# Optimization experiments

Hardware: AMD Instinct MI355X
Metric: run time of the kernel (lower is better)

Reference implementation:

```python
import jax, jax.numpy as jnp
import numpy as np

# dims
T, B, NB, P = 128, 8, 256, 16
N = NB * P            # 4096 neurons
E = 4096              # active block-edges (target_connectivity=16 per block)
# cfg constants
ACT_LR = 0.01         # homeostatic bias learning rate
SETPOINT = 0.1        # homeostatic activity setpoint
SYN_LR = 0.01         # synaptic learning rate
ALPHA = 0.01          # trophic map EMA alpha
MAX_NORM = 1.0        # per-block weight norm cap
DMAX = 0.1            # per-block delta norm cap
EPS = 1e-8


def setup_inputs() -> dict:
    key = jax.random.key(0)
    ks = jax.random.split(key, 10)
    return {
        "states": jax.random.normal(ks[0], (T, B, N), jnp.float32),
        "elig": jax.random.normal(ks[1], (T, B, N), jnp.float32),
        "act": jax.random.uniform(ks[2], (T, B, N), jnp.float32),
        "inv": jax.random.uniform(ks[3], (T, B, 1), jnp.float32),
        "var": jax.random.normal(ks[4], (T, B, N), jnp.float32),
        "weight_values": jax.random.normal(ks[5], (E, P, P), jnp.float32) * 0.1,
        "activity_bias": jax.random.normal(ks[6], (1, N), jnp.float32) * 0.01,
        "trophic_map": jax.random.uniform(ks[7], (NB, NB), jnp.float32),
        "weight_rows": jax.random.randint(ks[8], (E,), 0, NB, jnp.int32),
        "weight_cols": jax.random.randint(ks[9], (E,), 0, NB, jnp.int32),
        "active_blocks": jnp.ones((E,), jnp.bool_),
    }


def reference(states, elig, act, inv, var, weight_values, activity_bias,
              trophic_map, weight_rows, weight_cols, active_blocks):
    mask = active_blocks.astype(weight_values.dtype)  # [E]

    def step(carry, xs):
        W, bias, troph = carry
        s, e, a, iv, v = xs  # s,e,a,v: [B,N]; iv: [B,1]
        # 1) homeostatic bias update toward setpoint
        bias = bias + ACT_LR * jnp.mean((SETPOINT - a) * iv, axis=0, keepdims=True)
        # 2) modulated error signal with postsynaptic gain (1 - s^2)
        mod = v * (1.0 - s * s)                         # [B,N]
        eb = e.reshape(B, NB, P)                        # eligibility pre blocks
        mb = mod.reshape(B, NB, P)                      # modulated post blocks
        pre = eb[:, weight_cols]                        # [B,E,P] gather
        post = mb[:, weight_rows]                       # [B,E,P] gather
        ivb = iv[:, 0]                                  # [B]
        # 3) Hebbian outer product (norm-scaled, batch-averaged) minus Oja decay
        hebb = jnp.einsum('bei,bej,b->eij', post, pre, ivb) / B   # [E,P,P]
        post2 = jnp.einsum('bei,b->ei', post * post, ivb) / B     # [E,P]
        dw = hebb - post2[:, :, None] * W
        # clip per-block update norm (delta_max_norm)
        dn = jnp.sqrt(jnp.sum(dw * dw, axis=(1, 2), keepdims=True))
        dw = dw * jnp.minimum(1.0, DMAX / (dn + EPS))
        W = W + SYN_LR * dw * mask[:, None, None]
        # renormalize per-block weight norm (max_norm)
        wn = jnp.sqrt(jnp.sum(W * W, axis=(1, 2), keepdims=True))
        W = W * jnp.minimum(1.0, MAX_NORM / (wn + EPS))
        # 4) trophic support map EMA via scatter of per-edge update strength
        strength = jnp.sqrt(jnp.sum(dw * dw, axis=(1, 2)))         # [E]
        troph = (1.0 - ALPHA) * troph
        troph = troph.at[weight_rows, weight_cols].add(ALPHA * strength)
        return (W, bias, troph), None

    (W, bias, troph), _ = jax.lax.scan(
        step, (weight_values, activity_bias, trophic_map),
        (states, elig, act, inv, var))
    return W
```

## Files before the change

### kernel.cpp

```cpp
#include <hip/hip_runtime.h>


namespace {
constexpr int T = 128, B = 8, NB = 256, P = 16;
constexpr int N = NB * P;
constexpr int E = 4096;
constexpr int BN = B * N;
constexpr float SYN_LR = 0.01f;
constexpr float DMAX   = 0.1f;
}

typedef __attribute__((ext_vector_type(8))) short short8v;
typedef __attribute__((ext_vector_type(4))) float float4v;
typedef __attribute__((ext_vector_type(2))) float float2v;

#if defined(__HIP_DEVICE_COMPILE__)
#define MFMA_B16(A, Bv, C) \
  __builtin_amdgcn_mfma_f32_16x16x32_bf16((A), (Bv), (C), 0, 0, 0)
#else
static __device__ inline float4v MFMA_B16(short8v, short8v, float4v C) { return C; }
#endif

__device__ __forceinline__ uint32_t bf16_rne(float x) {
  const uint32_t u = __float_as_uint(x);
  return (u + 0x7fffu + ((u >> 16) & 1u)) >> 16;
}

template<int CTRL>
__device__ __forceinline__ float dpp_add(float v) {
  return v + __int_as_float(__builtin_amdgcn_update_dpp(
      0, __float_as_int(v), CTRL, 0xF, 0xF, true));
}
__device__ __forceinline__ float wave_total(float v) {
  v = dpp_add<0xB1>(v);
  v = dpp_add<0x4E>(v);
  v = dpp_add<0x141>(v);
  v = dpp_add<0x140>(v);
  v = dpp_add<0x142>(v);
  v = dpp_add<0x143>(v);
  return __int_as_float(__builtin_amdgcn_readlane(__float_as_int(v), 63));
}

__global__ __launch_bounds__(256)
void prepass2(const float* __restrict__ states,
              const float* __restrict__ var,
              const float* __restrict__ elig,
              const float* __restrict__ inv,
              uint4* __restrict__ postT,
              uint4* __restrict__ preT,
              float* __restrict__ postSq)
{
  const int t  = blockIdx.x >> 2;
  const int n4 = ((blockIdx.x & 3) << 8) | threadIdx.x;
  const int n0 = n4 * 4;
  const size_t base = (size_t)t * BN + n0;

  uint32_t ph[4][4], pl[4][4], qh[4][4];
  float sq[4] = {0.f, 0.f, 0.f, 0.f};
#pragma unroll
  for (int b = 0; b < 8; ++b) {
    const float sc = sqrtf(inv[t * B + b] * 0.125f);
    const float4 s4 = *reinterpret_cast<const float4*>(states + base + (size_t)b * N);
    const float4 v4 = *reinterpret_cast<const float4*>(var    + base + (size_t)b * N);
    const float4 e4 = *reinterpret_cast<const float4*>(elig   + base + (size_t)b * N);
    const float ss[4] = {s4.x, s4.y, s4.z, s4.w};
    const float vv[4] = {v4.x, v4.y, v4.z, v4.w};
    const float ee[4] = {e4.x, e4.y, e4.z, e4.w};
#pragma unroll
    for (int r = 0; r < 4; ++r) {
      float po = vv[r] * (1.0f - ss[r] * ss[r]) * sc;
      const float pr = ee[r] * sc;
      sq[r] = fmaf(po, po, sq[r]);
      po *= 0.25f;
      const uint32_t hp = bf16_rne(po);
      const uint32_t lp = bf16_rne(po - __uint_as_float(hp << 16));
      const uint32_t hq = bf16_rne(pr);
      if ((b & 1) == 0) {
        ph[r][b >> 1] = hp;  pl[r][b >> 1] = lp;  qh[r][b >> 1] = hq;
      } else {
        ph[r][b >> 1] |= hp << 16;  pl[r][b >> 1] |= lp << 16;
        qh[r][b >> 1] |= hq << 16;
      }
    }
  }
  const size_t row0 = (size_t)t * N + n0;
#pragma unroll
  for (int r = 0; r < 4; ++r) {
    const size_t row = row0 + r;
    postT[row * 2]     = make_uint4(ph[r][0], ph[r][1], ph[r][2], ph[r][3]);
    postT[row * 2 + 1] = make_uint4(pl[r][0], pl[r][1], pl[r][2], pl[r][3]);
    preT [row]         = make_uint4(qh[r][0], qh[r][1], qh[r][2], qh[r][3]);
  }
  *reinterpret_cast<float4*>(postSq + row0) = make_float4(sq[0], sq[1], sq[2], sq[3]);
}

__global__ __launch_bounds__(256)
void scan_mfma(const char* __restrict__ postT,
               const char* __restrict__ preT,
               const char* __restrict__ postSq,
               const float* __restrict__ Win,
               const int* __restrict__ rows,
               const int* __restrict__ cols,
               float* __restrict__ out)
{
  const int tid  = threadIdx.x;
  const int wv   = tid >> 6;
  const int lane = tid & 63;
  const int e    = blockIdx.x * 4 + wv;
  const int g    = lane >> 4;
  const int c    = lane & 15;
  const int roff = __builtin_amdgcn_readfirstlane(rows[e]) * P;
  const int coff = __builtin_amdgcn_readfirstlane(cols[e]) * P;

  const size_t wbase = (size_t)e * 256 + (size_t)(4 * g) * 16 + c;
  float2v w01 = { Win[wbase +  0], Win[wbase + 16] };
  float2v w23 = { Win[wbase + 32], Win[wbase + 48] };
  const float2v t2i = __builtin_elementwise_fma(w01, w01, w23 * w23);
  float wn2 = wave_total(t2i[0] + t2i[1]);

  const char* pA = postT  + (size_t)roff * 32;
  const char* pB = preT   + (size_t)coff * 16;
  const char* pS = postSq + (size_t)roff * 4;
  const int vA = c << 5;
  const int vB = c << 4;
  const int vS = g << 4;
  constexpr int SA = N * 32, SB = N * 16, SS = N * 4;

  const float4v zero4 = {0.f, 0.f, 0.f, 0.f};
  constexpr float DS = DMAX * SYN_LR;

#define LOADSLOT(i, OFF)                                           \
  short8v Ah##i = *(const short8v*)(pA + (OFF) * SA + vA);         \
  short8v Al##i = *(const short8v*)(pA + (OFF) * SA + vA + 16);    \
  short8v Bh##i = *(const short8v*)(pB + (OFF) * SB + vB);         \
  float4v sq##i = *(const float4v*)(pS + (OFF) * SS + vS);
  LOADSLOT(0, 0)
  LOADSLOT(1, 1)
  LOADSLOT(2, 2)
  LOADSLOT(3, 3)
#undef LOADSLOT
  pA += 4 * SA; pB += 4 * SB; pS += 4 * SS;

  float4v hebbA = MFMA_B16(Ah0, Bh0, MFMA_B16(Al0, Bh0, zero4));
  float4v hebbB;

#define BODY(AHn, BHn, ALn, SQc, AHc, ALc, BHc, HIN, HOUT, SOFF)              \
  {                                                                           \
    HOUT = MFMA_B16(AHn, BHn, MFMA_B16(ALn, BHn, zero4));                     \
    const float2v sq01 = __builtin_shufflevector(SQc, SQc, 0, 1);             \
    const float2v sq23 = __builtin_shufflevector(SQc, SQc, 2, 3);             \
    const float2v h01  = __builtin_shufflevector(HIN, HIN, 0, 1);             \
    const float2v h23  = __builtin_shufflevector(HIN, HIN, 2, 3);             \
    const float2v d01 = __builtin_elementwise_fma(-sq01, w01, h01);           \
    const float2v d23 = __builtin_elementwise_fma(-sq23, w23, h23);           \
    AHc = *(const short8v*)(pA + (SOFF) * SA + vA);                           \
    ALc = *(const short8v*)(pA + (SOFF) * SA + vA + 16);                      \
    BHc = *(const short8v*)(pB + (SOFF) * SB + vB);                           \
    SQc = *(const float4v*)(pS + (SOFF) * SS + vS);                           \
    const float2v dd2 = __builtin_elementwise_fma(d01, d01, d23 * d23);       \
    const float2v wd2 = __builtin_elementwise_fma(w01, d01, w23 * d23);       \
    const float ddt = wave_total(dd2[0] + dd2[1]);                            \
    const float wdt = wave_total(wd2[0] + wd2[1]);                            \
       \
    const float cl = fminf(SYN_LR, DS * __builtin_amdgcn_rsqf(ddt));          \
    const float ws = fmaxf(fmaf(cl, fmaf(cl, ddt, wdt + wdt), wn2), 0.0f);    \
    const float wcl = fminf(1.0f, __builtin_amdgcn_rsqf(ws));     \
    const float ccl = wcl * cl;                                               \
    const float2v wclv = { wcl, wcl };                                        \
    const float2v cclv = { ccl, ccl };                                        \
    w01 = __builtin_elementwise_fma(d01, cclv, w01 * wclv);                   \
    w23 = __builtin_elementwise_fma(d23, cclv, w23 * wclv);                   \
                \
    wn2 = fminf(ws, 1.0f);                                                    \
  }

  for (int t = 0; t < T; t += 4) {
    BODY(Ah1, Bh1, Al1, sq0, Ah0, Al0, Bh0, hebbA, hebbB, 0)
    BODY(Ah2, Bh2, Al2, sq1, Ah1, Al1, Bh1, hebbB, hebbA, 1)
    BODY(Ah3, Bh3, Al3, sq2, Ah2, Al2, Bh2, hebbA, hebbB, 2)
    BODY(Ah0, Bh0, Al0, sq3, Ah3, Al3, Bh3, hebbB, hebbA, 3)
    pA += 4 * SA; pB += 4 * SB; pS += 4 * SS;
  }
#undef BODY

  out[wbase +  0] = w01[0];
  out[wbase + 16] = w01[1];
  out[wbase + 32] = w23[0];
  out[wbase + 48] = w23[1];
}

__global__ __launch_bounds__(256)
void plasticity_scan_fb(const float* __restrict__ states,
                        const float* __restrict__ elig,
                        const float* __restrict__ inv,
                        const float* __restrict__ var,
                        const float* __restrict__ Win,
                        const int*   __restrict__ rows,
                        const int*   __restrict__ cols,
                        float*       __restrict__ out)
{
  __shared__ float ivs[T * B];
  __shared__ float postL[4][B * P];
  __shared__ float preL [4][B * P];

  const int tid = threadIdx.x;
  for (int k = tid; k < T * B; k += 256) ivs[k] = inv[k] * (1.0f / B);
  __syncthreads();

  const int wv   = tid >> 6;
  const int lane = tid & 63;
  const int e    = blockIdx.x * 4 + wv;
  const int irow = lane >> 2;
  const int jcol = (lane & 3) * 4;
  const int roff = rows[e] * P;
  const int coff = cols[e] * P;

  float4 w = *reinterpret_cast<const float4*>(Win + (size_t)e * 256 + lane * 4);

  const int k0 = lane, k1 = lane + 64;
  const int b0 = k0 >> 4, i0 = k0 & 15;
  const int b1 = k1 >> 4, i1 = k1 & 15;
  float* pL = postL[wv];
  float* qL = preL[wv];

  for (int t = 0; t < T; ++t) {
    const size_t base = (size_t)t * BN;
    {
      const size_t ga = base + (size_t)b0 * N + roff + i0;
      const size_t gb = base + (size_t)b1 * N + roff + i1;
      const float s0 = states[ga], v0 = var[ga];
      const float s1 = states[gb], v1 = var[gb];
      const size_t ha = base + (size_t)b0 * N + coff + i0;
      const size_t hb = base + (size_t)b1 * N + coff + i1;
      pL[k0] = v0 * (1.0f - s0 * s0);
      pL[k1] = v1 * (1.0f - s1 * s1);
      qL[k0] = elig[ha];
      qL[k1] = elig[hb];
    }
    float h0 = 0.f, h1 = 0.f, h2 = 0.f, h3 = 0.f, p2 = 0.f;
#pragma unroll
    for (int b = 0; b < B; ++b) {
      const float iv = ivs[t * B + b];
      const float pp = pL[b * 16 + irow];
      const float4 q = *reinterpret_cast<const float4*>(qL + b * 16 + jcol);
      const float pv = pp * iv;
      p2 = fmaf(pv, pp, p2);
      h0 = fmaf(pv, q.x, h0);
      h1 = fmaf(pv, q.y, h1);
      h2 = fmaf(pv, q.z, h2);
      h3 = fmaf(pv, q.w, h3);
    }
    float d0 = h0 - p2 * w.x;
    float d1 = h1 - p2 * w.y;
    float d2 = h2 - p2 * w.z;
    float d3 = h3 - p2 * w.w;
    float s = d0 * d0 + d1 * d1 + d2 * d2 + d3 * d3;
#pragma unroll
    for (int off = 32; off > 0; off >>= 1) s += __shfl_xor(s, off, 64);
    const float dn = sqrtf(s);
    const float cl = fminf(1.0f, DMAX / (dn + 1e-8f)) * SYN_LR;
    w.x = fmaf(cl, d0, w.x);
    w.y = fmaf(cl, d1, w.y);
    w.z = fmaf(cl, d2, w.z);
    w.w = fmaf(cl, d3, w.w);
    float ws = w.x * w.x + w.y * w.y + w.z * w.z + w.w * w.w;
#pragma unroll
    for (int off = 32; off > 0; off >>= 1) ws += __shfl_xor(ws, off, 64);
    const float wn = sqrtf(ws);
    const float wcl = fminf(1.0f, 1.0f / (wn + 1e-8f));
    w.x *= wcl; w.y *= wcl; w.z *= wcl; w.w *= wcl;
  }
  *reinterpret_cast<float4*>(out + (size_t)e * 256 + lane * 4) = w;
}

extern "C" void kernel_launch(void* const* d_in, const int* in_sizes, int n_in,
                              void* d_out, int out_size, void* d_ws, size_t ws_size,
                              hipStream_t stream) {
  const float* states = (const float*)d_in[0];
  const float* elig   = (const float*)d_in[1];
  const float* inv    = (const float*)d_in[3];
  const float* var    = (const float*)d_in[4];
  const float* Win    = (const float*)d_in[5];
  const int* rows     = (const int*)d_in[8];
  const int* cols     = (const int*)d_in[9];

  float* out = (float*)d_out;

  const size_t szA  = (size_t)T * N * 32;
  const size_t szB  = (size_t)T * N * 16;
  const size_t szS  = (size_t)T * N * 4;
  const size_t need = szA + szB + szS + 262144;
  if (ws_size >= need) {
    char* postT  = (char*)d_ws;
    char* preT   = postT + szA;
    char* postSq = preT + szB;
    prepass2<<<T * 4, 256, 0, stream>>>(states, var, elig, inv,
                                        (uint4*)postT, (uint4*)preT,
                                        (float*)postSq);
    scan_mfma<<<E / 4, 256, 0, stream>>>(postT, preT, postSq, Win,
                                         rows, cols, out);
  } else {
    plasticity_scan_fb<<<E / 4, 256, 0, stream>>>(states, elig, inv, var,
                                                  Win, rows, cols, out);
  }
}
```

Before: 89.47 us.

## Drop bf16 low-part split for post operand and fuse dual wave reductions

Removes the hi/lo bf16 split of the postsynaptic operand, so the prepass writes half as much post data and the scan does one MFMA per step instead of two, with half the post loads. Also merges the two per-step wave reductions into a single reduction using a permlane32 swap, cutting DPP instruction count in the serial dependency chain. The price is lower precision in the Hebbian term (plain bf16 instead of roughly fp32-accurate two-term bf16), which may affect accuracy over the 128-step scan.

```diff
diff --git a/kernel.cpp b/kernel.cpp
--- a/kernel.cpp
+++ b/kernel.cpp
@@ -13,12 +13,15 @@
 typedef __attribute__((ext_vector_type(8))) short short8v;
 typedef __attribute__((ext_vector_type(4))) float float4v;
 typedef __attribute__((ext_vector_type(2))) float float2v;
+typedef __attribute__((ext_vector_type(2))) int   int2v;
 
 #if defined(__HIP_DEVICE_COMPILE__)
 #define MFMA_B16(A, Bv, C) \
   __builtin_amdgcn_mfma_f32_16x16x32_bf16((A), (Bv), (C), 0, 0, 0)
+#define PERMSWAP(a, b) __builtin_amdgcn_permlane32_swap((a), (b), false, false)
 #else
 static __device__ inline float4v MFMA_B16(short8v, short8v, float4v C) { return C; }
+static __device__ inline int2v PERMSWAP(int, int) { return int2v{0, 0}; }
 #endif
 
 __device__ __forceinline__ uint32_t bf16_rne(float x) {
@@ -39,6 +42,18 @@
   v = dpp_add<0x142>(v);
   v = dpp_add<0x143>(v);
   return __int_as_float(__builtin_amdgcn_readlane(__float_as_int(v), 63));
+}
+__device__ __forceinline__ void wave_total2(float dd, float wd,
+                                            float& ddt, float& wdt) {
+  const int2v sw = PERMSWAP(__float_as_int(dd), __float_as_int(wd));
+  float u = __int_as_float(sw.x) + __int_as_float(sw.y);
+  u = dpp_add<0xB1>(u);
+  u = dpp_add<0x4E>(u);
+  u = dpp_add<0x141>(u);
+  u = dpp_add<0x140>(u);
+  u = dpp_add<0x142>(u);
+  ddt = __int_as_float(__builtin_amdgcn_readlane(__float_as_int(u), 31));
+  wdt = __int_as_float(__builtin_amdgcn_readlane(__float_as_int(u), 63));
 }
 
 __global__ __launch_bounds__(256)
@@ -55,7 +70,7 @@
   const int n0 = n4 * 4;
   const size_t base = (size_t)t * BN + n0;
 
-  uint32_t ph[4][4], pl[4][4], qh[4][4];
+  uint32_t ph[4][4], qh[4][4];
   float sq[4] = {0.f, 0.f, 0.f, 0.f};
 #pragma unroll
   for (int b = 0; b < 8; ++b) {
@@ -73,13 +88,11 @@
       sq[r] = fmaf(po, po, sq[r]);
       po *= 0.25f;
       const uint32_t hp = bf16_rne(po);
-      const uint32_t lp = bf16_rne(po - __uint_as_float(hp << 16));
       const uint32_t hq = bf16_rne(pr);
       if ((b & 1) == 0) {
-        ph[r][b >> 1] = hp;  pl[r][b >> 1] = lp;  qh[r][b >> 1] = hq;
+        ph[r][b >> 1] = hp;  qh[r][b >> 1] = hq;
       } else {
-        ph[r][b >> 1] |= hp << 16;  pl[r][b >> 1] |= lp << 16;
-        qh[r][b >> 1] |= hq << 16;
+        ph[r][b >> 1] |= hp << 16;  qh[r][b >> 1] |= hq << 16;
       }
     }
   }
@@ -87,9 +100,8 @@
 #pragma unroll
   for (int r = 0; r < 4; ++r) {
     const size_t row = row0 + r;
-    postT[row * 2]     = make_uint4(ph[r][0], ph[r][1], ph[r][2], ph[r][3]);
-    postT[row * 2 + 1] = make_uint4(pl[r][0], pl[r][1], pl[r][2], pl[r][3]);
-    preT [row]         = make_uint4(qh[r][0], qh[r][1], qh[r][2], qh[r][3]);
+    postT[row] = make_uint4(ph[r][0], ph[r][1], ph[r][2], ph[r][3]);
+    preT [row] = make_uint4(qh[r][0], qh[r][1], qh[r][2], qh[r][3]);
   }
   *reinterpret_cast<float4*>(postSq + row0) = make_float4(sq[0], sq[1], sq[2], sq[3]);
 }
@@ -118,20 +130,19 @@
   const float2v t2i = __builtin_elementwise_fma(w01, w01, w23 * w23);
   float wn2 = wave_total(t2i[0] + t2i[1]);
 
-  const char* pA = postT  + (size_t)roff * 32;
+  const char* pA = postT  + (size_t)roff * 16;
   const char* pB = preT   + (size_t)coff * 16;
   const char* pS = postSq + (size_t)roff * 4;
-  const int vA = c << 5;
+  const int vA = c << 4;
   const int vB = c << 4;
   const int vS = g << 4;
-  constexpr int SA = N * 32, SB = N * 16, SS = N * 4;
+  constexpr int SA = N * 16, SB = N * 16, SS = N * 4;
 
   const float4v zero4 = {0.f, 0.f, 0.f, 0.f};
   constexpr float DS = DMAX * SYN_LR;
 
 #define LOADSLOT(i, OFF)                                           \
   short8v Ah##i = *(const short8v*)(pA + (OFF) * SA + vA);         \
-  short8v Al##i = *(const short8v*)(pA + (OFF) * SA + vA + 16);    \
   short8v Bh##i = *(const short8v*)(pB + (OFF) * SB + vB);         \
   float4v sq##i = *(const float4v*)(pS + (OFF) * SS + vS);
   LOADSLOT(0, 0)
@@ -141,12 +152,12 @@
 #undef LOADSLOT
   pA += 4 * SA; pB += 4 * SB; pS += 4 * SS;
 
-  float4v hebbA = MFMA_B16(Ah0, Bh0, MFMA_B16(Al0, Bh0, zero4));
+  float4v hebbA = MFMA_B16(Ah0, Bh0, zero4);
   float4v hebbB;
 
-#define BODY(AHn, BHn, ALn, SQc, AHc, ALc, BHc, HIN, HOUT, SOFF)              \
+#define BODY(AHn, BHn, SQc, AHc, BHc, HIN, HOUT, SOFF)                        \
   {                                                                           \
-    HOUT = MFMA_B16(AHn, BHn, MFMA_B16(ALn, BHn, zero4));                     \
+    HOUT = MFMA_B16(AHn, BHn, zero4);                                         \
     const float2v sq01 = __builtin_shufflevector(SQc, SQc, 0, 1);             \
     const float2v sq23 = __builtin_shufflevector(SQc, SQc, 2, 3);             \
     const float2v h01  = __builtin_shufflevector(HIN, HIN, 0, 1);             \
@@ -154,13 +165,12 @@
     const float2v d01 = __builtin_elementwise_fma(-sq01, w01, h01);           \
     const float2v d23 = __builtin_elementwise_fma(-sq23, w23, h23);           \
     AHc = *(const short8v*)(pA + (SOFF) * SA + vA);                           \
-    ALc = *(const short8v*)(pA + (SOFF) * SA + vA + 16);                      \
     BHc = *(const short8v*)(pB + (SOFF) * SB + vB);                           \
     SQc = *(const float4v*)(pS + (SOFF) * SS + vS);                           \
     const float2v dd2 = __builtin_elementwise_fma(d01, d01, d23 * d23);       \
     const float2v wd2 = __builtin_elementwise_fma(w01, d01, w23 * d23);       \
-    const float ddt = wave_total(dd2[0] + dd2[1]);                            \
-    const float wdt = wave_total(wd2[0] + wd2[1]);                            \
+    float ddt, wdt;                                                           \
+    wave_total2(dd2[0] + dd2[1], wd2[0] + wd2[1], ddt, wdt);                  \
        \
     const float cl = fminf(SYN_LR, DS * __builtin_amdgcn_rsqf(ddt));          \
     const float ws = fmaxf(fmaf(cl, fmaf(cl, ddt, wdt + wdt), wn2), 0.0f);    \
@@ -175,10 +185,10 @@
   }
 
   for (int t = 0; t < T; t += 4) {
-    BODY(Ah1, Bh1, Al1, sq0, Ah0, Al0, Bh0, hebbA, hebbB, 0)
-    BODY(Ah2, Bh2, Al2, sq1, Ah1, Al1, Bh1, hebbB, hebbA, 1)
-    BODY(Ah3, Bh3, Al3, sq2, Ah2, Al2, Bh2, hebbA, hebbB, 2)
-    BODY(Ah0, Bh0, Al0, sq3, Ah3, Al3, Bh3, hebbB, hebbA, 3)
+    BODY(Ah1, Bh1, sq0, Ah0, Bh0, hebbA, hebbB, 0)
+    BODY(Ah2, Bh2, sq1, Ah1, Bh1, hebbB, hebbA, 1)
+    BODY(Ah3, Bh3, sq2, Ah2, Bh2, hebbA, hebbB, 2)
+    BODY(Ah0, Bh0, sq3, Ah3, Bh3, hebbB, hebbA, 3)
     pA += 4 * SA; pB += 4 * SB; pS += 4 * SS;
   }
 #undef BODY
@@ -286,7 +296,7 @@
 
   float* out = (float*)d_out;
 
-  const size_t szA  = (size_t)T * N * 32;
+  const size_t szA  = (size_t)T * N * 16;
   const size_t szB  = (size_t)T * N * 16;
   const size_t szS  = (size_t)T * N * 4;
   const size_t need = szA + szB + szS + 262144;
```

After: 76.03 us. -15.0%, faster.
